# Kernel optimization log

Hardware: AMD Instinct MI355X
Metric: run time of the kernel (lower is better)

Reference implementation:

```python
import jax, jax.numpy as jnp
import numpy as np
import math

B, S, D, H = 2, 2048, 1024, 16
HD = D // H  # head dim = 64


def _rope_tables():
    # RoFormer sinusoidal position embedding: one frequency per (even, odd) pair
    pos = jnp.arange(S, dtype=jnp.float32)[:, None]                # [S, 1]
    inv_freq = 1.0 / (10000.0 ** (jnp.arange(0, HD, 2, dtype=jnp.float32) / HD))  # [HD/2]
    ang = pos * inv_freq[None, :]                                   # [S, HD/2]
    sin = jnp.sin(ang)[None, None]                                  # [1,1,S,HD/2]
    cos = jnp.cos(ang)[None, None]
    return sin, cos


def setup_inputs() -> dict:
    key = jax.random.key(0)
    k0, k1, k2, k3 = jax.random.split(key, 4)
    scale = 1.0 / math.sqrt(D)
    sin, cos = _rope_tables()
    return {
        "hidden_states": jax.random.normal(k0, (B, S, D), dtype=jnp.float32),
        "Wq": jax.random.normal(k1, (D, D), dtype=jnp.float32) * scale,
        "Wk": jax.random.normal(k2, (D, D), dtype=jnp.float32) * scale,
        "Wv": jax.random.normal(k3, (D, D), dtype=jnp.float32) * scale,
        "sin": sin,
        "cos": cos,
    }


def _split_heads(x):
    # [B,S,D] -> [B,H,S,HD]
    b, s, _ = x.shape
    return x.reshape(b, s, H, HD).transpose(0, 2, 1, 3)


def _apply_rotary(x, sin, cos):
    # x: [B,H,S,HD]; sin/cos broadcast as [1,1,S,HD/2]
    x1 = x[..., 0::2]
    x2 = x[..., 1::2]
    out = jnp.stack([x1 * cos - x2 * sin, x2 * cos + x1 * sin], axis=-1)
    return out.reshape(x.shape)


def reference(hidden_states, Wq, Wk, Wv, sin, cos):
    q = _apply_rotary(_split_heads(hidden_states @ Wq), sin, cos)  # [B,H,S,HD]
    k = _apply_rotary(_split_heads(hidden_states @ Wk), sin, cos)
    v = _apply_rotary(_split_heads(hidden_states @ Wv), sin, cos)  # note: RoPE on V too, per source
    scores = jnp.einsum("bhqd,bhkd->bhqk", q, k) / math.sqrt(HD)   # [B,H,S,S]
    probs = jax.nn.softmax(scores, axis=-1)
    ctx = jnp.einsum("bhqk,bhkd->bhqd", probs, v)                   # [B,H,S,HD]
    return ctx.transpose(0, 2, 1, 3).reshape(hidden_states.shape[0], S, D)
```

## Files before the change

kernel.cpp:

```cpp
#include <hip/hip_runtime.h>

typedef unsigned short u16;
typedef unsigned short u16x8 __attribute__((ext_vector_type(8)));
typedef unsigned short u16x4 __attribute__((ext_vector_type(4)));
typedef __bf16 bf16x8_t __attribute__((ext_vector_type(8)));
typedef float floatx4 __attribute__((ext_vector_type(4)));

#define BATCH 2
#define S_LEN 2048
#define D_DIM 1024
#define NH    16
#define HD    64

__device__ __forceinline__ u16 f2b(float f) {
  union { float f; unsigned int i; } c; c.f = f;
  const unsigned int i = c.i;
  return (u16)((i + 0x7FFFu + ((i >> 16) & 1u)) >> 16);
}
__device__ __forceinline__ unsigned int fbits(float f) {
  union { float f; unsigned int i; } c; c.f = f; return c.i;
}
__device__ __forceinline__ bf16x8_t asbf(u16x8 v) {
  union { u16x8 u; bf16x8_t b; } c; c.u = v; return c.b;
}
__device__ __forceinline__ void load_lds16(const u16* g, u16* l) {
  __builtin_amdgcn_global_load_lds(
      (const __attribute__((address_space(1))) void*)g,
      (__attribute__((address_space(3))) void*)l, 16, 0, 0);
}

__device__ __attribute__((aligned(256))) u16 g_xb[(size_t)BATCH * S_LEN * D_DIM];
__device__ __attribute__((aligned(256))) u16 g_wt[3u * D_DIM * D_DIM];
__device__ __attribute__((aligned(256))) u16 g_qkv[3u * BATCH * S_LEN * D_DIM];

__global__ __launch_bounds__(256) void prep(const float* __restrict__ X,
                                            const float* __restrict__ Wq,
                                            const float* __restrict__ Wk,
                                            const float* __restrict__ Wv) {
  const int tid = threadIdx.x;
  const int z = blockIdx.y;
  if (z == 3) {
#pragma unroll
    for (int c = 0; c < 8; ++c) {
      const size_t i = (((size_t)c * 256 + blockIdx.x) * 256 + tid) * 8;
      floatx4 a = *(const floatx4*)(X + i);
      floatx4 b = *(const floatx4*)(X + i + 4);
      u16x8 o;
#pragma unroll
      for (int j = 0; j < 4; ++j) { o[j] = f2b(a[j]); o[4 + j] = f2b(b[j]); }
      *(u16x8*)(g_xb + i) = o;
    }
    return;
  }
  __shared__ u16 t[64][65];
  const float* W = (z == 0) ? Wq : (z == 1) ? Wk : Wv;
  u16* Wt = g_wt + (size_t)z * D_DIM * D_DIM;
  const int k0 = (blockIdx.x & 15) * 64;
  const int n0 = (blockIdx.x >> 4) * 64;
  const int rr = tid >> 4;
  const int cc = (tid & 15) * 4;
#pragma unroll
  for (int i = 0; i < 4; ++i) {
    const int r = rr + i * 16;
    floatx4 v = *(const floatx4*)(W + (size_t)(k0 + r) * D_DIM + n0 + cc);
    t[r][cc] = f2b(v[0]); t[r][cc + 1] = f2b(v[1]);
    t[r][cc + 2] = f2b(v[2]); t[r][cc + 3] = f2b(v[3]);
  }
  __syncthreads();
#pragma unroll
  for (int i = 0; i < 4; ++i) {
    const int r = rr + i * 16;
    u16x4 v;
    v[0] = t[cc][r]; v[1] = t[cc + 1][r]; v[2] = t[cc + 2][r]; v[3] = t[cc + 3][r];
    *(u16x4*)(Wt + (size_t)(n0 + r) * D_DIM + k0 + cc) = v;
  }
}

__global__ __launch_bounds__(256) void qkv_gemm(const float* __restrict__ sin_t,
                                                const float* __restrict__ cos_t) {
  __shared__ __attribute__((aligned(16))) u16 lds_a[128 * 32];
  __shared__ __attribute__((aligned(16))) u16 lds_b[128 * 32];
  const int tid = threadIdx.x;
  const int wv = tid >> 6;
  const int lane = tid & 63;
  const int lrow = lane & 15;
  const int quad = lane >> 4;
  const int wr = wv >> 1, wc = wv & 1;
  const int m0 = blockIdx.x * 128;
  const int n0 = blockIdx.y * 128;
  const int z = blockIdx.z;
  const bool vmode = (z == 2);
  const u16* Wz = g_wt + (size_t)z * (D_DIM * D_DIM);

  floatx4 acc[4][4] = {};

  const u16* gA = g_xb + (size_t)(m0 + wv * 32 + (lane >> 2)) * D_DIM + (lane & 3) * 8;
  const u16* gB = Wz   + (size_t)(n0 + wv * 32 + (lane >> 2)) * D_DIM + (lane & 3) * 8;
  u16* sA = &lds_a[(wv * 32) * 32];
  u16* sB = &lds_b[(wv * 32) * 32];

  const u16* Aarr = vmode ? lds_a : lds_b;
  const u16* Barr = vmode ? lds_b : lds_a;

  for (int k0 = 0; k0 < D_DIM; k0 += 32) {
    __syncthreads();
    load_lds16(gA + k0, sA);
    load_lds16(gA + (size_t)16 * D_DIM + k0, sA + 512);
    load_lds16(gB + k0, sB);
    load_lds16(gB + (size_t)16 * D_DIM + k0, sB + 512);
    __syncthreads();
    u16x8 af[4], bfr[4];
#pragma unroll
    for (int mi = 0; mi < 4; ++mi)
      af[mi] = *(const u16x8*)&Aarr[(wr * 64 + mi * 16 + lrow) * 32 + quad * 8];
#pragma unroll
    for (int ni = 0; ni < 4; ++ni)
      bfr[ni] = *(const u16x8*)&Barr[(wc * 64 + ni * 16 + lrow) * 32 + quad * 8];
#pragma unroll
    for (int mi = 0; mi < 4; ++mi)
#pragma unroll
      for (int ni = 0; ni < 4; ++ni)
        acc[mi][ni] = __builtin_amdgcn_mfma_f32_16x16x32_bf16(
            asbf(af[mi]), asbf(bfr[ni]), acc[mi][ni], 0, 0, 0);
  }

  if (!vmode) {
    const float qsc = (z == 0) ? 0.18033688011112042f : 1.0f;
    u16* outz = g_qkv + (size_t)z * (BATCH * S_LEN * D_DIM);
#pragma unroll
    for (int mi = 0; mi < 4; ++mi) {
      const int nf0 = n0 + wr * 64 + mi * 16 + quad * 4;
      const int h = nf0 >> 6, hd0 = nf0 & 63, i00 = hd0 >> 1;
#pragma unroll
      for (int ni = 0; ni < 4; ++ni) {
        const int sg = m0 + wc * 64 + ni * 16 + lrow;
        const int b = sg >> 11, srow = sg & 2047;
        const float c0 = cos_t[(size_t)srow * 32 + i00];
        const float s0 = sin_t[(size_t)srow * 32 + i00];
        const float c1 = cos_t[(size_t)srow * 32 + i00 + 1];
        const float s1 = sin_t[(size_t)srow * 32 + i00 + 1];
        const float v0 = acc[mi][ni][0], v1 = acc[mi][ni][1];
        const float v2 = acc[mi][ni][2], v3 = acc[mi][ni][3];
        u16x4 ov;
        ov[0] = f2b((v0 * c0 - v1 * s0) * qsc);
        ov[1] = f2b((v1 * c0 + v0 * s0) * qsc);
        ov[2] = f2b((v2 * c1 - v3 * s1) * qsc);
        ov[3] = f2b((v3 * c1 + v2 * s1) * qsc);
        *(u16x4*)(outz + ((size_t)(b * NH + h) * S_LEN + srow) * HD + hd0) = ov;
      }
    }
  } else {
    u16* outv = g_qkv + (size_t)2 * (BATCH * S_LEN * D_DIM);
#pragma unroll
    for (int mi = 0; mi < 4; ++mi) {
      const int s0g = m0 + wr * 64 + mi * 16 + quad * 4;
      const int b = s0g >> 11, sl = s0g & 2047;
#pragma unroll
      for (int ni = 0; ni < 4; ++ni) {
        const int nf = n0 + wc * 64 + ni * 16 + lrow;
        const int h = nf >> 6, hd = nf & 63, i0 = hd >> 1;
        const float sgn = (hd & 1) ? 1.f : -1.f;
        u16x4 ov;
#pragma unroll
        for (int r = 0; r < 4; ++r) {
          const int s = sl + r;
          const float c  = cos_t[(size_t)s * 32 + i0];
          const float sn = sin_t[(size_t)s * 32 + i0];
          const float v  = acc[mi][ni][r];
          const float vp = __shfl_xor(v, 1);
          ov[r] = f2b(v * c + sgn * sn * vp);
        }
        *(u16x4*)(outv + ((size_t)(b * NH + h) * HD + hd) * S_LEN + sl) = ov;
      }
    }
  }
}

__global__ __launch_bounds__(256) void flash_attn(float* __restrict__ out) {
  __shared__ __attribute__((aligned(16))) u16 lds_k[2][64 * 72];
  __shared__ __attribute__((aligned(16))) u16 lds_v[2][64 * 72];
  __shared__ __attribute__((aligned(16))) u16 lds_p[4][16 * 72];
  const int bh = blockIdx.x;
  const int qt = blockIdx.y;
  const int b = bh >> 4, h = bh & 15;
  const int tid = threadIdx.x, wv = tid >> 6, lane = tid & 63;
  const int lrow = lane & 15, quad = lane >> 4;
  const u16* Qb  = g_qkv + (size_t)bh * (S_LEN * HD);
  const u16* Kb  = g_qkv + (size_t)(BATCH * NH + bh) * (S_LEN * HD);
  const u16* VTb = g_qkv + (size_t)(2 * BATCH * NH + bh) * (S_LEN * HD);
  const int q0 = qt * 64 + wv * 16;

  u16x8 qf[2];
#pragma unroll
  for (int ks = 0; ks < 2; ++ks)
    qf[ks] = *(const u16x8*)(Qb + (size_t)(q0 + lrow) * HD + ks * 32 + quad * 8);

  floatx4 oacc[4] = {};
  float l_part = 0.f;

  const int sr = tid >> 3;
  const int sc = (tid & 7) * 8;
  u16* lp = lds_p[wv];

  u16x8 kreg[2], vreg[2];
#pragma unroll
  for (int i = 0; i < 2; ++i) {
    const int r = sr + i * 32;
    kreg[i] = *(const u16x8*)(Kb + (size_t)r * HD + sc);
    vreg[i] = *(const u16x8*)(VTb + (size_t)r * S_LEN + sc);
  }

  for (int t = 0; t < S_LEN / 64; ++t) {
    const int buf = t & 1;
#pragma unroll
    for (int i = 0; i < 2; ++i) {
      const int r = sr + i * 32;
      *(u16x8*)&lds_k[buf][r * 72 + sc] = kreg[i];
      *(u16x8*)&lds_v[buf][r * 72 + sc] = vreg[i];
    }
    __syncthreads();
    if (t + 1 < S_LEN / 64) {
      const int kv0n = (t + 1) * 64;
#pragma unroll
      for (int i = 0; i < 2; ++i) {
        const int r = sr + i * 32;
        kreg[i] = *(const u16x8*)(Kb + (size_t)(kv0n + r) * HD + sc);
        vreg[i] = *(const u16x8*)(VTb + (size_t)r * S_LEN + kv0n + sc);
      }
    }

    floatx4 sacc[4] = {};
#pragma unroll
    for (int nb = 0; nb < 4; ++nb)
#pragma unroll
      for (int ks = 0; ks < 2; ++ks) {
        u16x8 kf = *(const u16x8*)&lds_k[buf][(nb * 16 + lrow) * 72 + ks * 32 + quad * 8];
        sacc[nb] = __builtin_amdgcn_mfma_f32_16x16x32_bf16(
            asbf(kf), asbf(qf[ks]), sacc[nb], 0, 0, 0);
      }

#pragma unroll
    for (int nb = 0; nb < 4; ++nb) {
      const float p0 = __builtin_amdgcn_exp2f(sacc[nb][0]);
      const float p1 = __builtin_amdgcn_exp2f(sacc[nb][1]);
      const float p2 = __builtin_amdgcn_exp2f(sacc[nb][2]);
      const float p3 = __builtin_amdgcn_exp2f(sacc[nb][3]);
      l_part += (p0 + p1) + (p2 + p3);
      uint2 pk;
      pk.x = __byte_perm(fbits(p0), fbits(p1), 0x7632);
      pk.y = __byte_perm(fbits(p2), fbits(p3), 0x7632);
      *(uint2*)&lp[lrow * 72 + nb * 16 + quad * 4] = pk;
    }

#pragma unroll
    for (int ks = 0; ks < 2; ++ks) {
      u16x8 pf = *(const u16x8*)&lp[lrow * 72 + ks * 32 + quad * 8];
#pragma unroll
      for (int hb = 0; hb < 4; ++hb) {
        u16x8 vf = *(const u16x8*)&lds_v[buf][(hb * 16 + lrow) * 72 + ks * 32 + quad * 8];
        oacc[hb] = __builtin_amdgcn_mfma_f32_16x16x32_bf16(
            asbf(pf), asbf(vf), oacc[hb], 0, 0, 0);
      }
    }
  }

  float l = l_part;
  l += __shfl_xor(l, 16);
  l += __shfl_xor(l, 32);
  float linv[4];
#pragma unroll
  for (int r = 0; r < 4; ++r)
    linv[r] = 1.f / __shfl(l, quad * 4 + r);

#pragma unroll
  for (int hb = 0; hb < 4; ++hb) {
    const int hd = hb * 16 + lrow;
#pragma unroll
    for (int r = 0; r < 4; ++r) {
      const int q = q0 + quad * 4 + r;
      out[((size_t)(b * S_LEN) + q) * D_DIM + h * HD + hd] = oacc[hb][r] * linv[r];
    }
  }
}

extern "C" void kernel_launch(void* const* d_in, const int* in_sizes, int n_in,
                              void* d_out, int out_size, void* d_ws, size_t ws_size,
                              hipStream_t stream) {
  const float* X = (const float*)d_in[0];
  const float* sin_t = (const float*)d_in[4];
  const float* cos_t = (const float*)d_in[5];

  prep<<<dim3(256, 4), 256, 0, stream>>>(X, (const float*)d_in[1],
                                         (const float*)d_in[2],
                                         (const float*)d_in[3]);

  qkv_gemm<<<dim3(32, 8, 3), 256, 0, stream>>>(sin_t, cos_t);

  flash_attn<<<dim3(32, 32), 256, 0, stream>>>((float*)d_out);
}
```

Before: 196.6 us.

## Feed P directly from registers via 16x16x16 MFMA, drop LDS round-trip

Removes the per-wave LDS staging buffer for the softmax probabilities. The QK^T accumulator layout is reused directly as the A operand of 16x16x16 bf16 MFMAs, with V read in matching 4-element chunks. This eliminates an LDS write, a wait and a reread per tile, but doubles the number of PV MFMA instructions, each with half the K depth. It also wraps the MFMA phases in s_setprio to favour matrix issue across waves.

After: 193.2 us. About the same (-1.8%).

```diff
diff --git a/kernel.cpp b/kernel.cpp
--- a/kernel.cpp
+++ b/kernel.cpp
@@ -3,6 +3,7 @@
 typedef unsigned short u16;
 typedef unsigned short u16x8 __attribute__((ext_vector_type(8)));
 typedef unsigned short u16x4 __attribute__((ext_vector_type(4)));
+typedef short s16x4 __attribute__((ext_vector_type(4)));
 typedef __bf16 bf16x8_t __attribute__((ext_vector_type(8)));
 typedef float floatx4 __attribute__((ext_vector_type(4)));
 
@@ -22,6 +23,12 @@
 }
 __device__ __forceinline__ bf16x8_t asbf(u16x8 v) {
   union { u16x8 u; bf16x8_t b; } c; c.u = v; return c.b;
+}
+__device__ __forceinline__ s16x4 as4(uint2 v) {
+  union { uint2 u; s16x4 s; } c; c.u = v; return c.s;
+}
+__device__ __forceinline__ s16x4 as4u(u16x4 v) {
+  union { u16x4 u; s16x4 s; } c; c.u = v; return c.s;
 }
 __device__ __forceinline__ void load_lds16(const u16* g, u16* l) {
   __builtin_amdgcn_global_load_lds(
@@ -179,7 +186,6 @@
 __global__ __launch_bounds__(256) void flash_attn(float* __restrict__ out) {
   __shared__ __attribute__((aligned(16))) u16 lds_k[2][64 * 72];
   __shared__ __attribute__((aligned(16))) u16 lds_v[2][64 * 72];
-  __shared__ __attribute__((aligned(16))) u16 lds_p[4][16 * 72];
   const int bh = blockIdx.x;
   const int qt = blockIdx.y;
   const int b = bh >> 4, h = bh & 15;
@@ -200,7 +206,6 @@
 
   const int sr = tid >> 3;
   const int sc = (tid & 7) * 8;
-  u16* lp = lds_p[wv];
 
   u16x8 kreg[2], vreg[2];
 #pragma unroll
@@ -230,6 +235,7 @@
     }
 
     floatx4 sacc[4] = {};
+    __builtin_amdgcn_s_setprio(1);
 #pragma unroll
     for (int nb = 0; nb < 4; ++nb)
 #pragma unroll
@@ -238,7 +244,9 @@
         sacc[nb] = __builtin_amdgcn_mfma_f32_16x16x32_bf16(
             asbf(kf), asbf(qf[ks]), sacc[nb], 0, 0, 0);
       }
-
+    __builtin_amdgcn_s_setprio(0);
+
+    uint2 pk[4];
 #pragma unroll
     for (int nb = 0; nb < 4; ++nb) {
       const float p0 = __builtin_amdgcn_exp2f(sacc[nb][0]);
@@ -246,22 +254,22 @@
       const float p2 = __builtin_amdgcn_exp2f(sacc[nb][2]);
       const float p3 = __builtin_amdgcn_exp2f(sacc[nb][3]);
       l_part += (p0 + p1) + (p2 + p3);
-      uint2 pk;
-      pk.x = __byte_perm(fbits(p0), fbits(p1), 0x7632);
-      pk.y = __byte_perm(fbits(p2), fbits(p3), 0x7632);
-      *(uint2*)&lp[lrow * 72 + nb * 16 + quad * 4] = pk;
-    }
-
-#pragma unroll
-    for (int ks = 0; ks < 2; ++ks) {
-      u16x8 pf = *(const u16x8*)&lp[lrow * 72 + ks * 32 + quad * 8];
+      pk[nb].x = __byte_perm(fbits(p0), fbits(p1), 0x7632);
+      pk[nb].y = __byte_perm(fbits(p2), fbits(p3), 0x7632);
+    }
+
+    __builtin_amdgcn_s_setprio(1);
+#pragma unroll
+    for (int nb = 0; nb < 4; ++nb) {
+      const s16x4 pa = as4(pk[nb]);
 #pragma unroll
       for (int hb = 0; hb < 4; ++hb) {
-        u16x8 vf = *(const u16x8*)&lds_v[buf][(hb * 16 + lrow) * 72 + ks * 32 + quad * 8];
-        oacc[hb] = __builtin_amdgcn_mfma_f32_16x16x32_bf16(
-            asbf(pf), asbf(vf), oacc[hb], 0, 0, 0);
-      }
-    }
+        u16x4 vf = *(const u16x4*)&lds_v[buf][(hb * 16 + lrow) * 72 + nb * 16 + quad * 4];
+        oacc[hb] = __builtin_amdgcn_mfma_f32_16x16x16bf16_1k(
+            pa, as4u(vf), oacc[hb], 0, 0, 0);
+      }
+    }
+    __builtin_amdgcn_s_setprio(0);
   }
 
   float l = l_part;
```
